# Kernel tuning notes

Measured on AMD Instinct MI355X. Metric: run time of the kernel, lower is better.

## Reference

```python
import jax, jax.numpy as jnp
import numpy as np

B, H, M, D, MID, DV = 128, 8, 196, 128, 64, 128


def setup_inputs() -> dict:
    key0 = jax.random.key(0)
    ks = jax.random.split(key0, 12)
    query = jax.random.normal(ks[0], (B, H, D), dtype=jnp.float32)
    key = jax.random.normal(ks[1], (B, H, M, D), dtype=jnp.float32)
    att_mask = jax.random.randint(ks[2], (B, M), 0, 2).astype(jnp.float32)
    att_mask = att_mask.at[:, 0].set(1.0)  # guarantee each row has >=1 valid slot
    value1 = jax.random.normal(ks[3], (B, H, DV), dtype=jnp.float32)
    value2 = jax.random.normal(ks[4], (B, H, M, DV), dtype=jnp.float32)
    W_basic = jax.random.normal(ks[5], (D, MID), dtype=jnp.float32) * 0.05
    b_basic = jnp.zeros((MID,), dtype=jnp.float32)
    W_spatial = jax.random.normal(ks[6], (MID, 1), dtype=jnp.float32) * 0.05
    b_spatial = jnp.zeros((1,), dtype=jnp.float32)
    W_channel = jax.random.normal(ks[7], (MID, DV), dtype=jnp.float32) * 0.05
    b_channel = jnp.zeros((DV,), dtype=jnp.float32)
    return {
        'query': query, 'key': key, 'att_mask': att_mask,
        'value1': value1, 'value2': value2,
        'W_basic': W_basic, 'b_basic': b_basic,
        'W_spatial': W_spatial, 'b_spatial': b_spatial,
        'W_channel': W_channel, 'b_channel': b_channel,
    }


def reference(query, key, att_mask, value1, value2,
              W_basic, b_basic, W_spatial, b_spatial, W_channel, b_channel):
    # att_map: broadcast elementwise QK product  [B,H,M,D]
    att_map = query[..., None, :] * key
    # attention_basic: Linear + ReLU (Dropout is identity at eval)  [B,H,M,MID]
    h = jax.nn.relu(jnp.einsum('bhmd,de->bhme', att_map, W_basic) + b_basic)
    # masked mean-pool over regions  [B,H,MID]
    mask_ext = att_mask[:, None, :, None]  # [B,1,M,1]
    att_map_pool = jnp.sum(h * mask_ext, axis=-2) / jnp.sum(mask_ext, axis=-2)
    # spatial attention logits  [B,H,M]
    alpha_spatial = (jnp.einsum('bhme,eo->bhmo', h, W_spatial) + b_spatial)[..., 0]
    alpha_spatial = jnp.where(att_mask[:, None, :] == 0, -1e9, alpha_spatial)
    alpha_spatial = jax.nn.softmax(alpha_spatial, axis=-1)
    # weighted sum over regions  [B,H,DV]
    v2 = jnp.einsum('bhm,bhmv->bhv', alpha_spatial, value2)
    # channel gate  [B,H,DV]
    alpha_channel = jax.nn.sigmoid(jnp.einsum('bhe,ev->bhv', att_map_pool, W_channel) + b_channel)
    return value1 * v2 * alpha_channel
```

## Files before the change

### kernel.cpp

```cpp
#include <hip/hip_runtime.h>
#include <cstddef>

#define NBH  1024
#define Mm   196
#define Dd   128
#define MIDe 64
#define DVv  128

typedef __attribute__((ext_vector_type(8))) short bf16x8;
typedef __attribute__((ext_vector_type(4))) float f32x4;

__device__ __forceinline__ short f2bf(float x) {
    union { float f; unsigned u; } v; v.f = x;
    return (short)((v.u + 0x7FFFu + ((v.u >> 16) & 1u)) >> 16);
}

__device__ __forceinline__ float waveReduceSum(float v) {
#pragma unroll
    for (int off = 32; off > 0; off >>= 1) v += __shfl_xor(v, off, 64);
    return v;
}

__device__ __forceinline__ float waveReduceMax(float v) {
#pragma unroll
    for (int off = 32; off > 0; off >>= 1) v = fmaxf(v, __shfl_xor(v, off, 64));
    return v;
}

__global__ __launch_bounds__(256, 3)
void scatt_fused(const float* __restrict__ query,
                 const float* __restrict__ key,
                 const float* __restrict__ att_mask,
                 const float* __restrict__ value1,
                 const float* __restrict__ value2,
                 const float* __restrict__ W_basic,
                 const float* __restrict__ b_basic,
                 const float* __restrict__ W_spatial,
                 const float* __restrict__ b_spatial,
                 const float* __restrict__ W_channel,
                 const float* __restrict__ b_channel,
                 float* __restrict__ out)
{
    __shared__ float maskS[Mm];
    __shared__ float sS[Mm];
    __shared__ float poolPart[4][MIDe];
    __shared__ float poolS[MIDe];
    __shared__ float partS[8][DVv];
    __shared__ float redS[12];

    const int t    = threadIdx.x;
    const int lane = t & 63;
    const int w    = t >> 6;
    const int ln15 = lane & 15;
    const int q4   = lane >> 4;
    const int bh   = blockIdx.x;
    const int b    = bh >> 3;

    const float* __restrict__ keyB  = key      + (size_t)bh * Mm * Dd;
    const float* __restrict__ val2B = value2   + (size_t)bh * Mm * DVv;
    const float* __restrict__ qB    = query    + (size_t)bh * Dd;
    const float* __restrict__ maskB = att_mask + (size_t)b  * Mm;

    for (int i = t; i < Mm; i += 256) maskS[i] = maskB[i];

    bf16x8 bfr[4][4];
#pragma unroll
    for (int ks = 0; ks < 4; ++ks) {
        const int kb = ks * 32 + q4 * 8;
        float qv[8];
        *(float4*)&qv[0] = *(const float4*)(qB + kb);
        *(float4*)&qv[4] = *(const float4*)(qB + kb + 4);
#pragma unroll
        for (int nt = 0; nt < 4; ++nt) {
            const int n = nt * 16 + ln15;
            bf16x8 f;
#pragma unroll
            for (int j = 0; j < 8; ++j)
                f[j] = f2bf(qv[j] * W_basic[(kb + j) * MIDe + n]);
            bfr[ks][nt] = f;
        }
    }
    float bbv[4], wspv[4];
#pragma unroll
    for (int nt = 0; nt < 4; ++nt) {
        bbv[nt]  = b_basic[nt * 16 + ln15];
        wspv[nt] = W_spatial[nt * 16 + ln15];
    }
    const float bsp = b_spatial[0];
    float poolAcc[4] = {0.f, 0.f, 0.f, 0.f};

    __syncthreads();

    for (int mt = w; mt < 13; mt += 4) {
        f32x4 acc[4] = {f32x4{0,0,0,0}, f32x4{0,0,0,0},
                        f32x4{0,0,0,0}, f32x4{0,0,0,0}};
        const int mrow = min(mt * 16 + ln15, Mm - 1);
        const float* ap = keyB + (size_t)mrow * Dd + q4 * 8;
#pragma unroll
        for (int ks = 0; ks < 4; ++ks) {
            const float4 a0 = *(const float4*)(ap + ks * 32);
            const float4 a1 = *(const float4*)(ap + ks * 32 + 4);
            const bf16x8 af = { f2bf(a0.x), f2bf(a0.y), f2bf(a0.z), f2bf(a0.w),
                                f2bf(a1.x), f2bf(a1.y), f2bf(a1.z), f2bf(a1.w) };
#pragma unroll
            for (int nt = 0; nt < 4; ++nt)
                acc[nt] = __builtin_amdgcn_mfma_f32_16x16x32_bf16(
                              af, bfr[ks][nt], acc[nt], 0, 0, 0);
        }
#pragma unroll
        for (int r = 0; r < 4; ++r) {
            const int m = mt * 16 + q4 * 4 + r;
            const bool valid = m < Mm;
            const float msk = valid ? maskS[m] : 0.f;
            float srow = 0.f;
#pragma unroll
            for (int nt = 0; nt < 4; ++nt) {
                float hv = acc[nt][r] + bbv[nt];
                hv = hv > 0.f ? hv : 0.f;
                poolAcc[nt] = fmaf(hv, msk, poolAcc[nt]);
                srow = fmaf(hv, wspv[nt], srow);
            }
            srow += __shfl_xor(srow, 1, 64);
            srow += __shfl_xor(srow, 2, 64);
            srow += __shfl_xor(srow, 4, 64);
            srow += __shfl_xor(srow, 8, 64);
            if (valid && ln15 == 0) sS[m] = srow + bsp;
        }
    }
#pragma unroll
    for (int nt = 0; nt < 4; ++nt) {
        poolAcc[nt] += __shfl_xor(poolAcc[nt], 16, 64);
        poolAcc[nt] += __shfl_xor(poolAcc[nt], 32, 64);
    }
    if (lane < 16) {
#pragma unroll
        for (int nt = 0; nt < 4; ++nt)
            poolPart[w][nt * 16 + lane] = poolAcc[nt];
    }
    __syncthreads();

    const float myMask = (t < Mm) ? maskS[t] : 0.f;
    float myS = -3.0e38f;
    if (t < Mm) {
        myS = sS[t];
        if (myMask == 0.f) myS = -1.0e9f;
    }
    const float rmx = waveReduceMax(myS);
    if (lane == 0) redS[w] = rmx;
    __syncthreads();
    const float mx = fmaxf(fmaxf(redS[0], redS[1]), fmaxf(redS[2], redS[3]));
    const float ev = (t < Mm) ? __expf(myS - mx) : 0.f;
    const float s1 = waveReduceSum(ev);
    const float s2 = waveReduceSum(myMask);
    if (lane == 0) { redS[4 + w] = s1; redS[8 + w] = s2; }
    __syncthreads();
    const float denom = redS[4] + redS[5] + redS[6] + redS[7];
    const float cnt   = redS[8] + redS[9] + redS[10] + redS[11];
    if (t < Mm) sS[t] = ev / denom;
    if (t < MIDe)
        poolS[t] = (poolPart[0][t] + poolPart[1][t] + poolPart[2][t] + poolPart[3][t]) / cnt;
    __syncthreads();

    float chv = 0.f;
    if (t < DVv) {
        float a = b_channel[t];
#pragma unroll 8
        for (int e = 0; e < MIDe; ++e)
            a = fmaf(poolS[e], W_channel[e * DVv + t], a);
        chv = 1.f / (1.f + __expf(-a));
    }

    const int vq = t & 31;
    const int ms = t >> 5;
    float4 acc4 = make_float4(0.f, 0.f, 0.f, 0.f);
    for (int m = ms; m < Mm; m += 8) {
        const float a = sS[m];
        const float4 vv = *(const float4*)(val2B + (size_t)m * DVv + 4 * vq);
        acc4.x = fmaf(a, vv.x, acc4.x);
        acc4.y = fmaf(a, vv.y, acc4.y);
        acc4.z = fmaf(a, vv.z, acc4.z);
        acc4.w = fmaf(a, vv.w, acc4.w);
    }
    ((float4*)&partS[ms][0])[vq] = acc4;
    __syncthreads();

    if (t < DVv) {
        float v2v = 0.f;
#pragma unroll
        for (int i = 0; i < 8; ++i) v2v += partS[i][t];
        out[(size_t)bh * DVv + t] = value1[(size_t)bh * DVv + t] * v2v * chv;
    }
}

extern "C" void kernel_launch(void* const* d_in, const int* in_sizes, int n_in,
                              void* d_out, int out_size, void* d_ws, size_t ws_size,
                              hipStream_t stream) {
    const float* query     = (const float*)d_in[0];
    const float* key       = (const float*)d_in[1];
    const float* att_mask  = (const float*)d_in[2];
    const float* value1    = (const float*)d_in[3];
    const float* value2    = (const float*)d_in[4];
    const float* W_basic   = (const float*)d_in[5];
    const float* b_basic   = (const float*)d_in[6];
    const float* W_spatial = (const float*)d_in[7];
    const float* b_spatial = (const float*)d_in[8];
    const float* W_channel = (const float*)d_in[9];
    const float* b_channel = (const float*)d_in[10];
    float* out = (float*)d_out;

    scatt_fused<<<NBH, 256, 0, stream>>>(query, key, att_mask, value1, value2,
                                         W_basic, b_basic, W_spatial, b_spatial,
                                         W_channel, b_channel, out);
}
```

Before: 263.5 us.

## Build q-scaled bf16 weight fragments once in shared memory and batch key loads

Each wave used to compute the full q*W_basic bf16 B-fragments redundantly from global memory. Now the block computes them once cooperatively into a padded transposed LDS tile, and each wave reads its fragments from there. The key row loads for all k-slices are also issued up front before the MFMAs, launch bounds move to 4 blocks per CU, and the value2 reduction loop is unrolled. These add about 17KB of LDS and an extra barrier, and the higher occupancy target may cause register pressure or spills.

```diff
diff --git a/kernel.cpp b/kernel.cpp
--- a/kernel.cpp
+++ b/kernel.cpp
@@ -6,6 +6,7 @@
 #define Dd   128
 #define MIDe 64
 #define DVv  128
+#define WQLD 136
 
 typedef __attribute__((ext_vector_type(8))) short bf16x8;
 typedef __attribute__((ext_vector_type(4))) float f32x4;
@@ -27,7 +28,7 @@
     return v;
 }
 
-__global__ __launch_bounds__(256, 3)
+__global__ __launch_bounds__(256, 4)
 void scatt_fused(const float* __restrict__ query,
                  const float* __restrict__ key,
                  const float* __restrict__ att_mask,
@@ -41,6 +42,8 @@
                  const float* __restrict__ b_channel,
                  float* __restrict__ out)
 {
+    __shared__ short wqT[MIDe][WQLD];
+    __shared__ float qS[Dd];
     __shared__ float maskS[Mm];
     __shared__ float sS[Mm];
     __shared__ float poolPart[4][MIDe];
@@ -61,25 +64,33 @@
     const float* __restrict__ qB    = query    + (size_t)bh * Dd;
     const float* __restrict__ maskB = att_mask + (size_t)b  * Mm;
 
+    if (t < 32) ((float4*)qS)[t] = ((const float4*)qB)[t];
     for (int i = t; i < Mm; i += 256) maskS[i] = maskB[i];
+    __syncthreads();
+
+    {
+        const int e0 = lane;
+        const int d0 = w * 32;
+#pragma unroll
+        for (int c = 0; c < 4; ++c) {
+            short pk[8];
+#pragma unroll
+            for (int j = 0; j < 8; ++j) {
+                const int d = d0 + c * 8 + j;
+                pk[j] = f2bf(qS[d] * W_basic[d * MIDe + e0]);
+            }
+            *(bf16x8*)&wqT[e0][d0 + c * 8] = *(bf16x8*)pk;
+        }
+    }
+    __syncthreads();
 
     bf16x8 bfr[4][4];
 #pragma unroll
-    for (int ks = 0; ks < 4; ++ks) {
-        const int kb = ks * 32 + q4 * 8;
-        float qv[8];
-        *(float4*)&qv[0] = *(const float4*)(qB + kb);
-        *(float4*)&qv[4] = *(const float4*)(qB + kb + 4);
-#pragma unroll
-        for (int nt = 0; nt < 4; ++nt) {
-            const int n = nt * 16 + ln15;
-            bf16x8 f;
-#pragma unroll
-            for (int j = 0; j < 8; ++j)
-                f[j] = f2bf(qv[j] * W_basic[(kb + j) * MIDe + n]);
-            bfr[ks][nt] = f;
-        }
-    }
+    for (int ks = 0; ks < 4; ++ks)
+#pragma unroll
+        for (int nt = 0; nt < 4; ++nt)
+            bfr[ks][nt] = *(const bf16x8*)&wqT[nt * 16 + ln15][ks * 32 + q4 * 8];
+
     float bbv[4], wspv[4];
 #pragma unroll
     for (int nt = 0; nt < 4; ++nt) {
@@ -89,19 +100,23 @@
     const float bsp = b_spatial[0];
     float poolAcc[4] = {0.f, 0.f, 0.f, 0.f};
 
-    __syncthreads();
-
     for (int mt = w; mt < 13; mt += 4) {
+        const int mrow = min(mt * 16 + ln15, Mm - 1);
+        const float* ap = keyB + (size_t)mrow * Dd + q4 * 8;
+        float4 a0[4], a1[4];
+#pragma unroll
+        for (int ks = 0; ks < 4; ++ks) {
+            a0[ks] = *(const float4*)(ap + ks * 32);
+            a1[ks] = *(const float4*)(ap + ks * 32 + 4);
+        }
         f32x4 acc[4] = {f32x4{0,0,0,0}, f32x4{0,0,0,0},
                         f32x4{0,0,0,0}, f32x4{0,0,0,0}};
-        const int mrow = min(mt * 16 + ln15, Mm - 1);
-        const float* ap = keyB + (size_t)mrow * Dd + q4 * 8;
 #pragma unroll
         for (int ks = 0; ks < 4; ++ks) {
-            const float4 a0 = *(const float4*)(ap + ks * 32);
-            const float4 a1 = *(const float4*)(ap + ks * 32 + 4);
-            const bf16x8 af = { f2bf(a0.x), f2bf(a0.y), f2bf(a0.z), f2bf(a0.w),
-                                f2bf(a1.x), f2bf(a1.y), f2bf(a1.z), f2bf(a1.w) };
+            const bf16x8 af = { f2bf(a0[ks].x), f2bf(a0[ks].y),
+                                f2bf(a0[ks].z), f2bf(a0[ks].w),
+                                f2bf(a1[ks].x), f2bf(a1[ks].y),
+                                f2bf(a1[ks].z), f2bf(a1[ks].w) };
 #pragma unroll
             for (int nt = 0; nt < 4; ++nt)
                 acc[nt] = __builtin_amdgcn_mfma_f32_16x16x32_bf16(
@@ -173,6 +188,7 @@
     const int vq = t & 31;
     const int ms = t >> 5;
     float4 acc4 = make_float4(0.f, 0.f, 0.f, 0.f);
+#pragma unroll 5
     for (int m = ms; m < Mm; m += 8) {
         const float a = sS[m];
         const float4 vv = *(const float4*)(val2B + (size_t)m * DVv + 4 * vq);
```

Result: faster. 243.9 us (-7.4%).
